# Performance work log

Measured on AMD Instinct MI355X. Metric: run time of the kernel, lower is better.

The kernel has to match this reference:

```python
import jax, jax.numpy as jnp
import numpy as np
from jax import lax
from jax.scipy.special import logsumexp

B, T, C = 512, 512, 64


def setup_inputs() -> dict:
    key = jax.random.key(0)
    k1, k2, k3, k4, k5 = jax.random.split(key, 5)
    emissions = jax.random.normal(k1, (B, T, C), dtype=jnp.float32)
    tags = jax.random.randint(k2, (B, T), 0, C, dtype=jnp.int32)
    mask = jnp.ones((B, T), dtype=jnp.int32)
    transitions = jax.random.normal(k3, (C, C), dtype=jnp.float32)
    start_transitions = jax.random.normal(k4, (C,), dtype=jnp.float32)
    end_transitions = jax.random.normal(k5, (C,), dtype=jnp.float32)
    return {"emissions": emissions, "tags": tags, "mask": mask,
            "transitions": transitions, "start_transitions": start_transitions,
            "end_transitions": end_transitions}


def _log_partition(emissions, maskb, transitions, start_transitions, end_transitions):
    # forward algorithm: lp [B,C] carried over T-1 steps
    lp0 = start_transitions[None, :] + emissions[:, 0]  # [B,C]

    def step(lp, xs):
        emit_t, mask_t = xs  # [B,C], [B]
        # score[b,i,j] = lp[b,i] + trans[i,j] + emit[b,j]
        score = lp[:, :, None] + transitions[None, :, :] + emit_t[:, None, :]
        lp_next = logsumexp(score, axis=1)  # [B,C]
        lp = jnp.where(mask_t[:, None], lp_next, lp)
        return lp, None

    xs = (jnp.swapaxes(emissions[:, 1:], 0, 1), jnp.swapaxes(maskb[:, 1:], 0, 1))
    lp, _ = lax.scan(step, lp0, xs)
    return logsumexp(lp + end_transitions[None, :], axis=1)  # [B]


def _joint_score(emissions, tags, mask, maskb, transitions, start_transitions, end_transitions):
    b_idx = jnp.arange(emissions.shape[0])
    score0 = start_transitions[tags[:, 0]] + emissions[b_idx, 0, tags[:, 0]]  # [B]
    trans = transitions[tags[:, :-1], tags[:, 1:]]  # [B,T-1]
    emit = jnp.take_along_axis(emissions, tags[:, :, None], axis=2)[:, :, 0]  # [B,T]
    step_scores = jnp.where(maskb[:, 1:], trans + emit[:, 1:], 0.0)
    last_idx = jnp.sum(mask, axis=1).astype(jnp.int32) - 1
    last_tags = tags[b_idx, last_idx]
    return score0 + jnp.sum(step_scores, axis=1) + end_transitions[last_tags]


def reference(emissions, tags, mask, transitions, start_transitions, end_transitions):
    maskb = mask.astype(bool)
    log_denominator = _log_partition(emissions, maskb, transitions, start_transitions, end_transitions)
    log_numerator = _joint_score(emissions, tags, mask, maskb, transitions, start_transitions, end_transitions)
    return jnp.mean(log_denominator - log_numerator)
```

## Files before the change

kernel.cpp:

```cpp
#include <hip/hip_runtime.h>

#define Bn 512
#define Tn 512
#define Cn 64


template <int CTRL>
__device__ __forceinline__ float fmax_dpp(const float v) {
    const int o = __builtin_amdgcn_update_dpp(__float_as_int(v), __float_as_int(v),
                                              CTRL, 0xF, 0xF, false);
    return fmaxf(v, __int_as_float(o));
}

__device__ __forceinline__ float wave_max64(float v) {
    v = fmax_dpp<0x0B1>(v);
    v = fmax_dpp<0x04E>(v);
    v = fmax_dpp<0x141>(v);
    v = fmax_dpp<0x140>(v);
    v = fmax_dpp<0x142>(v);
    v = fmax_dpp<0x143>(v);
    return __int_as_float(__builtin_amdgcn_readlane(__float_as_int(v), 63));
}

__global__ __launch_bounds__(64) void crf_half_kernel(
    const float* __restrict__ emissions,
    const int*   __restrict__ tags,
    const int*   __restrict__ mask,
    const float* __restrict__ transitions,
    const float* __restrict__ start_t,
    const float* __restrict__ end_t,
    float*       __restrict__ ws_alpha,
    float*       __restrict__ ws_beta,
    float*       __restrict__ ws_lsF,
    float*       __restrict__ ws_lsB,
    float*       __restrict__ ws_num)
{
    const int  blk = blockIdx.x;
    const bool fwd = blk < Bn;
    const int  bt  = blk & (Bn - 1);
    const int  j   = threadIdx.x;

    const float* em  = emissions + (size_t)bt * Tn * Cn + j;
    const float* em0 = emissions + (size_t)bt * Tn * Cn;
    const int*   mk  = mask + bt * Tn;
    const int*   tg  = tags + bt * Tn;

    if (fwd) {
        float nsum = 0.f;
        int   mcnt = 0;
        for (int t = j; t < Tn; t += 64) {
            const int tag_t = tg[t];
            const int m_t   = mk[t];
            mcnt += m_t;
            if (t >= 1 && m_t) {
                const int tag_p = tg[t - 1];
                nsum += transitions[tag_p * Cn + tag_t] + em0[t * Cn + tag_t];
            }
        }
#pragma unroll
        for (int off = 32; off > 0; off >>= 1) {
            nsum += __shfl_xor(nsum, off, 64);
            mcnt += __shfl_xor(mcnt, off, 64);
        }

        float w[Cn];
#pragma unroll
        for (int i = 0; i < Cn; ++i) w[i] = __expf(transitions[i * Cn + j]);

        float lp0 = start_t[j] + em[0];
        const float m0 = wave_max64(lp0);
        float log_scale = m0;
        float a_self = __expf(lp0 - m0);

        float cur_e[4];
        int   cur_m[4];
#pragma unroll
        for (int k = 0; k < 4; ++k) {
            cur_e[k] = em[(size_t)(1 + k) * Cn];
            cur_m[k] = mk[1 + k];
        }

        for (int g = 0; g < 64; ++g) {
            float nxt_e[4];
            int   nxt_m[4];
#pragma unroll
            for (int k = 0; k < 4; ++k) {
                const int t = 4 * g + 5 + k;
                nxt_e[k] = em[(size_t)t * Cn];
                nxt_m[k] = mk[t];
            }
            float ex[4];
#pragma unroll
            for (int k = 0; k < 4; ++k) ex[k] = __expf(cur_e[k]);

#pragma unroll
            for (int k = 0; k < 4; ++k) {
                float au[Cn];
#pragma unroll
                for (int i = 0; i < Cn; ++i)
                    au[i] = __int_as_float(
                        __builtin_amdgcn_readlane(__float_as_int(a_self), i));

                float acc0 = 0.f, acc1 = 0.f, acc2 = 0.f, acc3 = 0.f;
#pragma unroll
                for (int i = 0; i < Cn; i += 4) {
                    acc0 = fmaf(au[i + 0], w[i + 0], acc0);
                    acc1 = fmaf(au[i + 1], w[i + 1], acc1);
                    acc2 = fmaf(au[i + 2], w[i + 2], acc2);
                    acc3 = fmaf(au[i + 3], w[i + 3], acc3);
                }
                float s = ((acc0 + acc1) + (acc2 + acc3)) * ex[k];
                if (!cur_m[k]) s = a_self;
                if (k == 3) {
                    const float mx = wave_max64(s);
                    s *= __builtin_amdgcn_rcpf(mx);
                    log_scale += __logf(mx);
                }
                a_self = s;
            }
#pragma unroll
            for (int k = 0; k < 4; ++k) {
                cur_e[k] = nxt_e[k];
                cur_m[k] = nxt_m[k];
            }
        }

        ws_alpha[bt * Cn + j] = a_self;
        if (j == 0) {
            ws_lsF[bt] = log_scale;
            const int t0 = tg[0];
            const int tl = tg[mcnt - 1];
            ws_num[bt] = start_t[t0] + em0[t0] + nsum + end_t[tl];
        }
    } else {
        float w[Cn];
#pragma unroll
        for (int i = 0; i < Cn; ++i) w[i] = __expf(transitions[j * Cn + i]);

        float lp0 = end_t[j];
        const float m0 = wave_max64(lp0);
        float log_scale = m0;
        float b_self = __expf(lp0 - m0);

        float cur_e[4];
        int   cur_m[4];
#pragma unroll
        for (int k = 0; k < 4; ++k) {
            const int u = Tn - 1 - k;
            cur_e[k] = em[(size_t)u * Cn];
            cur_m[k] = mk[u];
        }

        for (int g = 0; g < 64; ++g) {
            float nxt_e[4];
            int   nxt_m[4];
#pragma unroll
            for (int k = 0; k < 4; ++k) {
                const int u = Tn - 5 - 4 * g - k;
                nxt_e[k] = em[(size_t)u * Cn];
                nxt_m[k] = mk[u];
            }
            float ex[4];
#pragma unroll
            for (int k = 0; k < 4; ++k) ex[k] = __expf(cur_e[k]);

#pragma unroll
            for (int k = 0; k < 4; ++k) {
                const int s_idx = 4 * g + k;
                if (s_idx < Tn / 2 - 1) {
                    const float wv = b_self * ex[k];
                    float au[Cn];
#pragma unroll
                    for (int i = 0; i < Cn; ++i)
                        au[i] = __int_as_float(
                            __builtin_amdgcn_readlane(__float_as_int(wv), i));

                    float acc0 = 0.f, acc1 = 0.f, acc2 = 0.f, acc3 = 0.f;
#pragma unroll
                    for (int i = 0; i < Cn; i += 4) {
                        acc0 = fmaf(au[i + 0], w[i + 0], acc0);
                        acc1 = fmaf(au[i + 1], w[i + 1], acc1);
                        acc2 = fmaf(au[i + 2], w[i + 2], acc2);
                        acc3 = fmaf(au[i + 3], w[i + 3], acc3);
                    }
                    float s = ((acc0 + acc1) + (acc2 + acc3));
                    if (!cur_m[k]) s = b_self;
                    if (k == 3) {
                        const float mx = wave_max64(s);
                        s *= __builtin_amdgcn_rcpf(mx);
                        log_scale += __logf(mx);
                    }
                    b_self = s;
                }
            }
#pragma unroll
            for (int k = 0; k < 4; ++k) {
                cur_e[k] = nxt_e[k];
                cur_m[k] = nxt_m[k];
            }
        }

        ws_beta[bt * Cn + j] = b_self;
        if (j == 0) ws_lsB[bt] = log_scale;
    }
}

__global__ __launch_bounds__(64) void crf_combine_kernel(
    const float* __restrict__ ws_alpha,
    const float* __restrict__ ws_beta,
    const float* __restrict__ ws_lsF,
    const float* __restrict__ ws_lsB,
    const float* __restrict__ ws_num,
    float*       __restrict__ out)
{
    const int bt = blockIdx.x;
    const int j  = threadIdx.x;
    float v = ws_alpha[bt * Cn + j] * ws_beta[bt * Cn + j];
#pragma unroll
    for (int off = 32; off > 0; off >>= 1) v += __shfl_xor(v, off, 64);
    if (j == 0) {
        const float denom = ws_lsF[bt] + ws_lsB[bt] + __logf(v);
        atomicAdd(out, (denom - ws_num[bt]) * (1.0f / Bn));
    }
}

__global__ void crf_zero_kernel(float* out) { out[0] = 0.f; }

extern "C" void kernel_launch(void* const* d_in, const int* in_sizes, int n_in,
                              void* d_out, int out_size, void* d_ws, size_t ws_size,
                              hipStream_t stream)
{
    const float* emissions   = (const float*)d_in[0];
    const int*   tags        = (const int*)d_in[1];
    const int*   mask        = (const int*)d_in[2];
    const float* transitions = (const float*)d_in[3];
    const float* start_t     = (const float*)d_in[4];
    const float* end_t       = (const float*)d_in[5];

    float* ws       = (float*)d_ws;
    float* ws_alpha = ws;
    float* ws_beta  = ws_alpha + Bn * Cn;
    float* ws_lsF   = ws_beta + Bn * Cn;
    float* ws_lsB   = ws_lsF + Bn;
    float* ws_num   = ws_lsB + Bn;

    crf_zero_kernel<<<1, 1, 0, stream>>>((float*)d_out);
    crf_half_kernel<<<2 * Bn, Cn, 0, stream>>>(emissions, tags, mask, transitions,
                                               start_t, end_t,
                                               ws_alpha, ws_beta, ws_lsF, ws_lsB, ws_num);
    crf_combine_kernel<<<Bn, Cn, 0, stream>>>(ws_alpha, ws_beta, ws_lsF, ws_lsB,
                                              ws_num, (float*)d_out);
}
```

Baseline: 173.0 us.

## Broadcast state via LDS vector loads and packed FMA instead of readlane

Replaces the 64 per-step readlanes, which broadcast the scaled alpha/beta vector across the wave, with a write to a double-buffered LDS array followed by 16-byte broadcast reads. The dot product now uses packed two-wide FMAs on float2 vectors, and the renormalisation multiply is deferred into the next step's k==0 multiply. This aims to cut scalar readlane serialization and halve FMA issue count. The cost is LDS round-trip latency on the serial recurrence, plus reliance on wave_barrier alone for intra-wave ordering.

```diff
diff --git a/kernel.cpp b/kernel.cpp
--- a/kernel.cpp
+++ b/kernel.cpp
@@ -4,6 +4,9 @@
 #define Tn 512
 #define Cn 64
 
+
+typedef float f2 __attribute__((ext_vector_type(2)));
+typedef float f4 __attribute__((ext_vector_type(4)));
 
 template <int CTRL>
 __device__ __forceinline__ float fmax_dpp(const float v) {
@@ -40,6 +43,8 @@
     const int  bt  = blk & (Bn - 1);
     const int  j   = threadIdx.x;
 
+    __shared__ __align__(16) float abuf[2][Cn];
+
     const float* em  = emissions + (size_t)bt * Tn * Cn + j;
     const float* em0 = emissions + (size_t)bt * Tn * Cn;
     const int*   mk  = mask + bt * Tn;
@@ -63,14 +68,18 @@
             mcnt += __shfl_xor(mcnt, off, 64);
         }
 
-        float w[Cn];
-#pragma unroll
-        for (int i = 0; i < Cn; ++i) w[i] = __expf(transitions[i * Cn + j]);
+        f2 wv[32];
+#pragma unroll
+        for (int p = 0; p < 32; ++p) {
+            wv[p][0] = __expf(transitions[(2 * p)     * Cn + j]);
+            wv[p][1] = __expf(transitions[(2 * p + 1) * Cn + j]);
+        }
 
         float lp0 = start_t[j] + em[0];
         const float m0 = wave_max64(lp0);
         float log_scale = m0;
         float a_self = __expf(lp0 - m0);
+        float c_pend = 1.0f;
 
         float cur_e[4];
         int   cur_m[4];
@@ -95,25 +104,35 @@
 
 #pragma unroll
             for (int k = 0; k < 4; ++k) {
-                float au[Cn];
-#pragma unroll
-                for (int i = 0; i < Cn; ++i)
-                    au[i] = __int_as_float(
-                        __builtin_amdgcn_readlane(__float_as_int(a_self), i));
-
-                float acc0 = 0.f, acc1 = 0.f, acc2 = 0.f, acc3 = 0.f;
-#pragma unroll
-                for (int i = 0; i < Cn; i += 4) {
-                    acc0 = fmaf(au[i + 0], w[i + 0], acc0);
-                    acc1 = fmaf(au[i + 1], w[i + 1], acc1);
-                    acc2 = fmaf(au[i + 2], w[i + 2], acc2);
-                    acc3 = fmaf(au[i + 3], w[i + 3], acc3);
-                }
-                float s = ((acc0 + acc1) + (acc2 + acc3)) * ex[k];
+                abuf[k & 1][j] = a_self;
+                __builtin_amdgcn_wave_barrier();
+
+                const f4* ap = (const f4*)abuf[k & 1];
+                f2 facc0 = {0.f, 0.f}, facc1 = {0.f, 0.f};
+                f2 facc2 = {0.f, 0.f}, facc3 = {0.f, 0.f};
+#pragma unroll
+                for (int p = 0; p < 16; ++p) {
+                    const f4 q = ap[p];
+                    const f2 lo = {q.x, q.y};
+                    const f2 hi = {q.z, q.w};
+                    if ((p & 1) == 0) {
+                        facc0 = __builtin_elementwise_fma(lo, wv[2 * p],     facc0);
+                        facc1 = __builtin_elementwise_fma(hi, wv[2 * p + 1], facc1);
+                    } else {
+                        facc2 = __builtin_elementwise_fma(lo, wv[2 * p],     facc2);
+                        facc3 = __builtin_elementwise_fma(hi, wv[2 * p + 1], facc3);
+                    }
+                }
+                const f2 rr = (facc0 + facc2) + (facc1 + facc3);
+                float s = (rr.x + rr.y) * ex[k];
                 if (!cur_m[k]) s = a_self;
+                if (k == 0) {
+                    s *= c_pend;
+                    c_pend = 1.0f;
+                }
                 if (k == 3) {
                     const float mx = wave_max64(s);
-                    s *= __builtin_amdgcn_rcpf(mx);
+                    c_pend = __builtin_amdgcn_rcpf(mx);
                     log_scale += __logf(mx);
                 }
                 a_self = s;
@@ -125,6 +144,7 @@
             }
         }
 
+        a_self *= c_pend;
         ws_alpha[bt * Cn + j] = a_self;
         if (j == 0) {
             ws_lsF[bt] = log_scale;
@@ -133,14 +153,18 @@
             ws_num[bt] = start_t[t0] + em0[t0] + nsum + end_t[tl];
         }
     } else {
-        float w[Cn];
-#pragma unroll
-        for (int i = 0; i < Cn; ++i) w[i] = __expf(transitions[j * Cn + i]);
+        f2 wv[32];
+#pragma unroll
+        for (int p = 0; p < 32; ++p) {
+            wv[p][0] = __expf(transitions[j * Cn + 2 * p]);
+            wv[p][1] = __expf(transitions[j * Cn + 2 * p + 1]);
+        }
 
         float lp0 = end_t[j];
         const float m0 = wave_max64(lp0);
         float log_scale = m0;
         float b_self = __expf(lp0 - m0);
+        float c_pend = 1.0f;
 
         float cur_e[4];
         int   cur_m[4];
@@ -168,26 +192,36 @@
             for (int k = 0; k < 4; ++k) {
                 const int s_idx = 4 * g + k;
                 if (s_idx < Tn / 2 - 1) {
-                    const float wv = b_self * ex[k];
-                    float au[Cn];
-#pragma unroll
-                    for (int i = 0; i < Cn; ++i)
-                        au[i] = __int_as_float(
-                            __builtin_amdgcn_readlane(__float_as_int(wv), i));
-
-                    float acc0 = 0.f, acc1 = 0.f, acc2 = 0.f, acc3 = 0.f;
-#pragma unroll
-                    for (int i = 0; i < Cn; i += 4) {
-                        acc0 = fmaf(au[i + 0], w[i + 0], acc0);
-                        acc1 = fmaf(au[i + 1], w[i + 1], acc1);
-                        acc2 = fmaf(au[i + 2], w[i + 2], acc2);
-                        acc3 = fmaf(au[i + 3], w[i + 3], acc3);
-                    }
-                    float s = ((acc0 + acc1) + (acc2 + acc3));
+                    const float wval = b_self * ex[k];
+                    abuf[k & 1][j] = wval;
+                    __builtin_amdgcn_wave_barrier();
+
+                    const f4* ap = (const f4*)abuf[k & 1];
+                    f2 facc0 = {0.f, 0.f}, facc1 = {0.f, 0.f};
+                    f2 facc2 = {0.f, 0.f}, facc3 = {0.f, 0.f};
+#pragma unroll
+                    for (int p = 0; p < 16; ++p) {
+                        const f4 q = ap[p];
+                        const f2 lo = {q.x, q.y};
+                        const f2 hi = {q.z, q.w};
+                        if ((p & 1) == 0) {
+                            facc0 = __builtin_elementwise_fma(lo, wv[2 * p],     facc0);
+                            facc1 = __builtin_elementwise_fma(hi, wv[2 * p + 1], facc1);
+                        } else {
+                            facc2 = __builtin_elementwise_fma(lo, wv[2 * p],     facc2);
+                            facc3 = __builtin_elementwise_fma(hi, wv[2 * p + 1], facc3);
+                        }
+                    }
+                    const f2 rr = (facc0 + facc2) + (facc1 + facc3);
+                    float s = rr.x + rr.y;
                     if (!cur_m[k]) s = b_self;
+                    if (k == 0) {
+                        s *= c_pend;
+                        c_pend = 1.0f;
+                    }
                     if (k == 3) {
                         const float mx = wave_max64(s);
-                        s *= __builtin_amdgcn_rcpf(mx);
+                        c_pend = __builtin_amdgcn_rcpf(mx);
                         log_scale += __logf(mx);
                     }
                     b_self = s;
@@ -200,6 +234,7 @@
             }
         }
 
+        b_self *= c_pend;
         ws_beta[bt * Cn + j] = b_self;
         if (j == 0) ws_lsB[bt] = log_scale;
     }
```

New measurement: 225.7 us. 1.3x slower.

## Batch 16 sequences per wave and run CRF forward/backward recursion on bf16 MFMA

Applied to the files above, without the earlier changes.

Replaces the per-sequence readlane/FMA matrix-vector recursion with a batched 16x64 by 64x64 product using bf16 MFMA instructions. The exponentiated transition matrix is split into hi and lo bf16 parts to recover precision, with alpha staged through LDS between steps. The numerator computation moves into the combine kernel, and the output zeroing is folded into the main kernel, removing one launch. This cuts the 64-readlane-per-step serial cost and launches far fewer waves, at the price of bf16 rounding of alpha, LDS round trips every step, and lower occupancy (64 waves).

```diff
diff --git a/kernel.cpp b/kernel.cpp
--- a/kernel.cpp
+++ b/kernel.cpp
@@ -3,228 +3,455 @@
 #define Bn 512
 #define Tn 512
 #define Cn 64
-
+#define NCH 16
+#define NGRP (Bn / NCH)
+#define LDP 20
+
+
+typedef float f4    __attribute__((ext_vector_type(4)));
+typedef short bfrag __attribute__((ext_vector_type(8)));
+typedef unsigned int u32x4 __attribute__((ext_vector_type(4)));
+
+static __device__ __forceinline__ unsigned int pkbf16(float a, float b) {
+    unsigned int r;
+    asm("v_cvt_pk_bf16_f32 %0, %1, %2" : "=v"(r) : "v"(a), "v"(b));
+    return r;
+}
 
 template <int CTRL>
-__device__ __forceinline__ float fmax_dpp(const float v) {
+static __device__ __forceinline__ float fmax_dpp(const float v) {
     const int o = __builtin_amdgcn_update_dpp(__float_as_int(v), __float_as_int(v),
                                               CTRL, 0xF, 0xF, false);
     return fmaxf(v, __int_as_float(o));
 }
-
-__device__ __forceinline__ float wave_max64(float v) {
+static __device__ __forceinline__ float rowmax16(float v) {
     v = fmax_dpp<0x0B1>(v);
     v = fmax_dpp<0x04E>(v);
     v = fmax_dpp<0x141>(v);
     v = fmax_dpp<0x140>(v);
-    v = fmax_dpp<0x142>(v);
-    v = fmax_dpp<0x143>(v);
-    return __int_as_float(__builtin_amdgcn_readlane(__float_as_int(v), 63));
-}
-
-__global__ __launch_bounds__(64) void crf_half_kernel(
+    return v;
+}
+static __device__ __forceinline__ f4 mfma16(bfrag a, bfrag b, f4 c) {
+    return __builtin_amdgcn_mfma_f32_16x16x32_bf16(a, b, c, 0, 0, 0);
+}
+
+__global__ __launch_bounds__(64)
+__attribute__((amdgpu_waves_per_eu(1, 1)))
+void crf_mfma_kernel(const float* __restrict__ emissions,
+                     const int*   __restrict__ mask,
+                     const float* __restrict__ transitions,
+                     const float* __restrict__ start_t,
+                     const float* __restrict__ end_t,
+                     float*       __restrict__ ws_alpha,
+                     float*       __restrict__ ws_beta,
+                     float*       __restrict__ ws_lsF,
+                     float*       __restrict__ ws_lsB,
+                     float*       __restrict__ out)
+{
+    const int  blk = blockIdx.x;
+    const bool fwd = blk < NGRP;
+    const int  b0  = (fwd ? blk : blk - NGRP) * NCH;
+    const int  l   = threadIdx.x;
+    const int  lg  = l >> 4;
+    const int  lo4 = l & 15;
+
+    if (blk == 0 && l == 0) out[0] = 0.f;
+
+    __shared__ __align__(16) float lT[Cn * Cn];
+    __shared__ __align__(16) float lA[2][Cn * LDP];
+    __shared__ float sc[NCH];
+
+    {
+        const f4* T4  = (const f4*)transitions;
+        f4*       lT4 = (f4*)lT;
+#pragma unroll
+        for (int q = 0; q < 16; ++q) lT4[q * 64 + l] = T4[q * 64 + l];
+    }
+    __builtin_amdgcn_wave_barrier();
+
+    bfrag whi[4][2], wlo[4][2];
+#pragma unroll
+    for (int n0 = 0; n0 < 4; ++n0)
+#pragma unroll
+        for (int kh = 0; kh < 2; ++kh) {
+            float wv[8];
+#pragma unroll
+            for (int ii = 0; ii < 8; ++ii) {
+                const int kk = kh * 32 + lg * 8 + ii;
+                const int jj = n0 * 16 + lo4;
+                wv[ii] = __expf(fwd ? lT[kk * Cn + jj] : lT[jj * Cn + kk]);
+            }
+            u32x4 H, L;
+#pragma unroll
+            for (int p = 0; p < 4; ++p) {
+                const unsigned int h = pkbf16(wv[2*p], wv[2*p+1]);
+                const float h0 = __uint_as_float((h & 0xffffu) << 16);
+                const float h1 = __uint_as_float(h & 0xffff0000u);
+                H[p] = h;
+                L[p] = pkbf16(wv[2*p] - h0, wv[2*p+1] - h1);
+            }
+            whi[n0][kh] = __builtin_bit_cast(bfrag, H);
+            wlo[n0][kh] = __builtin_bit_cast(bfrag, L);
+        }
+
+    const f4* em4 = (const f4*)(emissions + (size_t)(b0 + lo4) * Tn * Cn + lg * 8);
+    float ls[4];
+    bfrag a0, a1;
+    const f4 zz = {0.f, 0.f, 0.f, 0.f};
+
+    if (fwd) {
+        {
+            float v[16];
+#pragma unroll
+            for (int z = 0; z < 4; ++z) {
+                const f4 e = em4[(z >> 1) * 8 + (z & 1)];
+#pragma unroll
+                for (int q = 0; q < 4; ++q)
+                    v[z*4+q] = start_t[(z>>1)*32 + lg*8 + (z&1)*4 + q] + e[q];
+            }
+            float mx = v[0];
+#pragma unroll
+            for (int i2 = 1; i2 < 16; ++i2) mx = fmaxf(mx, v[i2]);
+            mx = fmaxf(mx, __int_as_float(__builtin_amdgcn_ds_swizzle(__float_as_int(mx), 0x401F)));
+            mx = fmaxf(mx, __shfl_xor(mx, 32, 64));
+            u32x4 A0, A1;
+#pragma unroll
+            for (int p = 0; p < 4; ++p) {
+                A0[p] = pkbf16(__expf(v[2*p]   - mx), __expf(v[2*p+1]   - mx));
+                A1[p] = pkbf16(__expf(v[8+2*p] - mx), __expf(v[8+2*p+1] - mx));
+            }
+            a0 = __builtin_bit_cast(bfrag, A0);
+            a1 = __builtin_bit_cast(bfrag, A1);
+            if (l < NCH) sc[l] = mx;
+        }
+        __builtin_amdgcn_wave_barrier();
+#pragma unroll
+        for (int r = 0; r < 4; ++r) ls[r] = sc[4*lg + r];
+
+        f4  eq0[4], eq1[4];
+        int mv0, mv1;
+#pragma unroll
+        for (int z = 0; z < 4; ++z) {
+            eq1[z] = em4[1*16 + (z>>1)*8 + (z&1)];
+            eq0[z] = em4[2*16 + (z>>1)*8 + (z&1)];
+        }
+        mv1 = 1; if (l < NCH) mv1 = mask[(b0 + l) * Tn + 1];
+        mv0 = 1; if (l < NCH) mv0 = mask[(b0 + l) * Tn + 2];
+
+        unsigned long long mwlast = ~0ull;
+
+#pragma unroll 1
+        for (int t = 1; t <= 256; ++t) {
+            const int par = t & 1;
+            const f4 pfa = em4[(t+2)*16 + 0];
+            const f4 pfb = em4[(t+2)*16 + 1];
+            const f4 pfc = em4[(t+2)*16 + 8];
+            const f4 pfd = em4[(t+2)*16 + 9];
+            int pfm = 1; if (l < NCH) pfm = mask[(b0 + l) * Tn + (t + 2)];
+
+            f4 acc0 = mfma16(a0, whi[0][0], zz);
+            f4 acc1 = mfma16(a0, whi[1][0], zz);
+            f4 acc2 = mfma16(a0, whi[2][0], zz);
+            f4 acc3 = mfma16(a0, whi[3][0], zz);
+            acc0 = mfma16(a1, whi[0][1], acc0);
+            acc1 = mfma16(a1, whi[1][1], acc1);
+            acc2 = mfma16(a1, whi[2][1], acc2);
+            acc3 = mfma16(a1, whi[3][1], acc3);
+            acc0 = mfma16(a0, wlo[0][0], acc0);
+            acc1 = mfma16(a0, wlo[1][0], acc1);
+            acc2 = mfma16(a0, wlo[2][0], acc2);
+            acc3 = mfma16(a0, wlo[3][0], acc3);
+            acc0 = mfma16(a1, wlo[0][1], acc0);
+            acc1 = mfma16(a1, wlo[1][1], acc1);
+            acc2 = mfma16(a1, wlo[2][1], acc2);
+            acc3 = mfma16(a1, wlo[3][1], acc3);
+
+            const unsigned long long mw = __ballot((par ? mv1 : mv0) != 0);
+            const bool all1 = (mw == ~0ull);
+            mwlast = mw;
+
+            if ((t & 3) == 0) {
+#pragma unroll
+                for (int r = 0; r < 4; ++r) {
+                    float mr = fmaxf(fmaxf(acc0[r], acc1[r]), fmaxf(acc2[r], acc3[r]));
+                    mr = rowmax16(mr);
+                    float scl = __builtin_amdgcn_rcpf(mr);
+                    float lga = __logf(mr);
+                    if (!all1) {
+                        const bool fz = !((mw >> (4*lg + r)) & 1);
+                        scl = fz ? 1.0f : scl;
+                        lga = fz ? 0.0f : lga;
+                    }
+                    ls[r] += lga;
+                    acc0[r] *= scl; acc1[r] *= scl; acc2[r] *= scl; acc3[r] *= scl;
+                }
+            }
+
+            *(f4*)&lA[par][(     lo4) * LDP + 4*lg] = acc0;
+            *(f4*)&lA[par][(16 + lo4) * LDP + 4*lg] = acc1;
+            *(f4*)&lA[par][(32 + lo4) * LDP + 4*lg] = acc2;
+            *(f4*)&lA[par][(48 + lo4) * LDP + 4*lg] = acc3;
+            __builtin_amdgcn_wave_barrier();
+
+            if (t != 256) {
+                float ex[16];
+#pragma unroll
+                for (int z = 0; z < 4; ++z) {
+                    const f4 e = par ? eq1[z] : eq0[z];
+#pragma unroll
+                    for (int q = 0; q < 4; ++q) ex[z*4+q] = __expf(e[q]);
+                }
+                u32x4 NA0, NA1;
+#pragma unroll
+                for (int p = 0; p < 4; ++p) {
+                    const float f0 = lA[par][(     lg*8 + 2*p    ) * LDP + lo4] * ex[2*p];
+                    const float f1 = lA[par][(     lg*8 + 2*p + 1) * LDP + lo4] * ex[2*p+1];
+                    const float f2 = lA[par][(32 + lg*8 + 2*p    ) * LDP + lo4] * ex[8+2*p];
+                    const float f3 = lA[par][(32 + lg*8 + 2*p + 1) * LDP + lo4] * ex[8+2*p+1];
+                    NA0[p] = pkbf16(f0, f1);
+                    NA1[p] = pkbf16(f2, f3);
+                }
+                if (!all1) {
+                    const bool fz = !((mw >> lo4) & 1);
+                    const u32x4 O0 = __builtin_bit_cast(u32x4, a0);
+                    const u32x4 O1 = __builtin_bit_cast(u32x4, a1);
+#pragma unroll
+                    for (int p = 0; p < 4; ++p) {
+                        NA0[p] = fz ? O0[p] : NA0[p];
+                        NA1[p] = fz ? O1[p] : NA1[p];
+                    }
+                }
+                a0 = __builtin_bit_cast(bfrag, NA0);
+                a1 = __builtin_bit_cast(bfrag, NA1);
+                if (par) { eq1[0]=pfa; eq1[1]=pfb; eq1[2]=pfc; eq1[3]=pfd; mv1 = pfm; }
+                else     { eq0[0]=pfa; eq0[1]=pfb; eq0[2]=pfc; eq0[3]=pfd; mv0 = pfm; }
+            }
+        }
+
+        __builtin_amdgcn_wave_barrier();
+#pragma unroll
+        for (int s = 0; s < 16; ++s) {
+            const int i2 = (s >> 3) * 32 + lg * 8 + (s & 7);
+            ws_alpha[(size_t)(b0 + lo4) * Cn + i2] = lA[0][i2 * LDP + lo4];
+        }
+        if (mwlast != ~0ull) {
+            asm volatile("s_waitcnt vmcnt(0)" ::: "memory");
+            const bool fz = !((mwlast >> lo4) & 1);
+            if (fz) {
+                const u32x4 U0 = __builtin_bit_cast(u32x4, a0);
+                const u32x4 U1 = __builtin_bit_cast(u32x4, a1);
+#pragma unroll
+                for (int s = 0; s < 16; ++s) {
+                    const int kh = s >> 3, ii = s & 7;
+                    const unsigned int w = (kh == 0) ? U0[ii >> 1] : U1[ii >> 1];
+                    const float av = __uint_as_float(((w >> (16 * (ii & 1))) & 0xffffu) << 16);
+                    const f4 e = (s < 8) ? ((ii < 4) ? eq0[0] : eq0[1])
+                                         : ((ii < 4) ? eq0[2] : eq0[3]);
+                    const float ev = e[ii & 3];
+                    const int i2 = kh * 32 + lg * 8 + ii;
+                    ws_alpha[(size_t)(b0 + lo4) * Cn + i2] = av * __expf(0.f - ev);
+                }
+            }
+        }
+        if (lo4 == 0) {
+#pragma unroll
+            for (int r = 0; r < 4; ++r) ws_lsF[b0 + 4*lg + r] = ls[r];
+        }
+    } else {
+        {
+            float v[16], bv[16];
+#pragma unroll
+            for (int z = 0; z < 4; ++z) {
+                const f4 e = em4[511*16 + (z>>1)*8 + (z&1)];
+#pragma unroll
+                for (int q = 0; q < 4; ++q) {
+                    const int i2 = (z>>1)*32 + lg*8 + (z&1)*4 + q;
+                    bv[z*4+q] = end_t[i2];
+                    v[z*4+q]  = bv[z*4+q] + e[q];
+                }
+            }
+            float mx = v[0];
+#pragma unroll
+            for (int i2 = 1; i2 < 16; ++i2) mx = fmaxf(mx, v[i2]);
+            mx = fmaxf(mx, __int_as_float(__builtin_amdgcn_ds_swizzle(__float_as_int(mx), 0x401F)));
+            mx = fmaxf(mx, __shfl_xor(mx, 32, 64));
+            u32x4 A0, A1;
+#pragma unroll
+            for (int p = 0; p < 4; ++p) {
+                A0[p] = pkbf16(__expf(v[2*p]   - mx), __expf(v[2*p+1]   - mx));
+                A1[p] = pkbf16(__expf(v[8+2*p] - mx), __expf(v[8+2*p+1] - mx));
+            }
+            a0 = __builtin_bit_cast(bfrag, A0);
+            a1 = __builtin_bit_cast(bfrag, A1);
+            if (l < NCH) sc[l] = mx;
+#pragma unroll
+            for (int s = 0; s < 16; ++s) {
+                const int i2 = (s >> 3) * 32 + lg * 8 + (s & 7);
+                lA[1][i2 * LDP + lo4] = __expf(bv[s] - mx);
+            }
+        }
+        __builtin_amdgcn_wave_barrier();
+#pragma unroll
+        for (int r = 0; r < 4; ++r) ls[r] = sc[4*lg + r];
+
+        f4  eq0[4], eq1[4];
+        int mv0, mv1;
+#pragma unroll
+        for (int z = 0; z < 4; ++z) {
+            eq0[z] = em4[510*16 + (z>>1)*8 + (z&1)];
+            eq1[z] = em4[509*16 + (z>>1)*8 + (z&1)];
+        }
+        mv0 = 1; if (l < NCH) mv0 = mask[(b0 + l) * Tn + 511];
+        mv1 = 1; if (l < NCH) mv1 = mask[(b0 + l) * Tn + 510];
+
+#pragma unroll 1
+        for (int s = 0; s < 255; ++s) {
+            const int par = s & 1;
+            const f4 pfa = em4[(508 - s)*16 + 0];
+            const f4 pfb = em4[(508 - s)*16 + 1];
+            const f4 pfc = em4[(508 - s)*16 + 8];
+            const f4 pfd = em4[(508 - s)*16 + 9];
+            int pfm = 1; if (l < NCH) pfm = mask[(b0 + l) * Tn + (509 - s)];
+
+            f4 acc0 = mfma16(a0, whi[0][0], zz);
+            f4 acc1 = mfma16(a0, whi[1][0], zz);
+            f4 acc2 = mfma16(a0, whi[2][0], zz);
+            f4 acc3 = mfma16(a0, whi[3][0], zz);
+            acc0 = mfma16(a1, whi[0][1], acc0);
+            acc1 = mfma16(a1, whi[1][1], acc1);
+            acc2 = mfma16(a1, whi[2][1], acc2);
+            acc3 = mfma16(a1, whi[3][1], acc3);
+            acc0 = mfma16(a0, wlo[0][0], acc0);
+            acc1 = mfma16(a0, wlo[1][0], acc1);
+            acc2 = mfma16(a0, wlo[2][0], acc2);
+            acc3 = mfma16(a0, wlo[3][0], acc3);
+            acc0 = mfma16(a1, wlo[0][1], acc0);
+            acc1 = mfma16(a1, wlo[1][1], acc1);
+            acc2 = mfma16(a1, wlo[2][1], acc2);
+            acc3 = mfma16(a1, wlo[3][1], acc3);
+
+            const unsigned long long mw = __ballot((par ? mv1 : mv0) != 0);
+            const bool all1 = (mw == ~0ull);
+
+            if ((s & 3) == 3) {
+#pragma unroll
+                for (int r = 0; r < 4; ++r) {
+                    float mr = fmaxf(fmaxf(acc0[r], acc1[r]), fmaxf(acc2[r], acc3[r]));
+                    mr = rowmax16(mr);
+                    float scl = __builtin_amdgcn_rcpf(mr);
+                    float lga = __logf(mr);
+                    if (!all1) {
+                        const bool fz = !((mw >> (4*lg + r)) & 1);
+                        scl = fz ? 1.0f : scl;
+                        lga = fz ? 0.0f : lga;
+                    }
+                    ls[r] += lga;
+                    acc0[r] *= scl; acc1[r] *= scl; acc2[r] *= scl; acc3[r] *= scl;
+                }
+            }
+
+            if (!all1) {
+                const f4 pv0 = *(const f4*)&lA[par ^ 1][(     lo4) * LDP + 4*lg];
+                const f4 pv1 = *(const f4*)&lA[par ^ 1][(16 + lo4) * LDP + 4*lg];
+                const f4 pv2 = *(const f4*)&lA[par ^ 1][(32 + lo4) * LDP + 4*lg];
+                const f4 pv3 = *(const f4*)&lA[par ^ 1][(48 + lo4) * LDP + 4*lg];
+#pragma unroll
+                for (int r = 0; r < 4; ++r) {
+                    const bool fz = !((mw >> (4*lg + r)) & 1);
+                    acc0[r] = fz ? pv0[r] : acc0[r];
+                    acc1[r] = fz ? pv1[r] : acc1[r];
+                    acc2[r] = fz ? pv2[r] : acc2[r];
+                    acc3[r] = fz ? pv3[r] : acc3[r];
+                }
+            }
+            *(f4*)&lA[par][(     lo4) * LDP + 4*lg] = acc0;
+            *(f4*)&lA[par][(16 + lo4) * LDP + 4*lg] = acc1;
+            *(f4*)&lA[par][(32 + lo4) * LDP + 4*lg] = acc2;
+            *(f4*)&lA[par][(48 + lo4) * LDP + 4*lg] = acc3;
+            __builtin_amdgcn_wave_barrier();
+
+            if (s != 254) {
+                float ex[16];
+#pragma unroll
+                for (int z = 0; z < 4; ++z) {
+                    const f4 e = par ? eq1[z] : eq0[z];
+#pragma unroll
+                    for (int q = 0; q < 4; ++q) ex[z*4+q] = __expf(e[q]);
+                }
+                u32x4 NA0, NA1;
+#pragma unroll
+                for (int p = 0; p < 4; ++p) {
+                    const float f0 = lA[par][(     lg*8 + 2*p    ) * LDP + lo4] * ex[2*p];
+                    const float f1 = lA[par][(     lg*8 + 2*p + 1) * LDP + lo4] * ex[2*p+1];
+                    const float f2 = lA[par][(32 + lg*8 + 2*p    ) * LDP + lo4] * ex[8+2*p];
+                    const float f3 = lA[par][(32 + lg*8 + 2*p + 1) * LDP + lo4] * ex[8+2*p+1];
+                    NA0[p] = pkbf16(f0, f1);
+                    NA1[p] = pkbf16(f2, f3);
+                }
+                a0 = __builtin_bit_cast(bfrag, NA0);
+                a1 = __builtin_bit_cast(bfrag, NA1);
+                if (par) { eq1[0]=pfa; eq1[1]=pfb; eq1[2]=pfc; eq1[3]=pfd; mv1 = pfm; }
+                else     { eq0[0]=pfa; eq0[1]=pfb; eq0[2]=pfc; eq0[3]=pfd; mv0 = pfm; }
+            }
+        }
+
+        __builtin_amdgcn_wave_barrier();
+#pragma unroll
+        for (int s = 0; s < 16; ++s) {
+            const int i2 = (s >> 3) * 32 + lg * 8 + (s & 7);
+            ws_beta[(size_t)(b0 + lo4) * Cn + i2] = lA[0][i2 * LDP + lo4];
+        }
+        if (lo4 == 0) {
+#pragma unroll
+            for (int r = 0; r < 4; ++r) ws_lsB[b0 + 4*lg + r] = ls[r];
+        }
+    }
+}
+
+__global__ __launch_bounds__(64) void crf_combine_kernel(
     const float* __restrict__ emissions,
     const int*   __restrict__ tags,
     const int*   __restrict__ mask,
     const float* __restrict__ transitions,
     const float* __restrict__ start_t,
     const float* __restrict__ end_t,
-    float*       __restrict__ ws_alpha,
-    float*       __restrict__ ws_beta,
-    float*       __restrict__ ws_lsF,
-    float*       __restrict__ ws_lsB,
-    float*       __restrict__ ws_num)
-{
-    const int  blk = blockIdx.x;
-    const bool fwd = blk < Bn;
-    const int  bt  = blk & (Bn - 1);
-    const int  j   = threadIdx.x;
-
-    const float* em  = emissions + (size_t)bt * Tn * Cn + j;
-    const float* em0 = emissions + (size_t)bt * Tn * Cn;
-    const int*   mk  = mask + bt * Tn;
-    const int*   tg  = tags + bt * Tn;
-
-    if (fwd) {
-        float nsum = 0.f;
-        int   mcnt = 0;
-        for (int t = j; t < Tn; t += 64) {
-            const int tag_t = tg[t];
-            const int m_t   = mk[t];
-            mcnt += m_t;
-            if (t >= 1 && m_t) {
-                const int tag_p = tg[t - 1];
-                nsum += transitions[tag_p * Cn + tag_t] + em0[t * Cn + tag_t];
-            }
-        }
-#pragma unroll
-        for (int off = 32; off > 0; off >>= 1) {
-            nsum += __shfl_xor(nsum, off, 64);
-            mcnt += __shfl_xor(mcnt, off, 64);
-        }
-
-        float w[Cn];
-#pragma unroll
-        for (int i = 0; i < Cn; ++i) w[i] = __expf(transitions[i * Cn + j]);
-
-        float lp0 = start_t[j] + em[0];
-        const float m0 = wave_max64(lp0);
-        float log_scale = m0;
-        float a_self = __expf(lp0 - m0);
-
-        float cur_e[4];
-        int   cur_m[4];
-#pragma unroll
-        for (int k = 0; k < 4; ++k) {
-            cur_e[k] = em[(size_t)(1 + k) * Cn];
-            cur_m[k] = mk[1 + k];
-        }
-
-        for (int g = 0; g < 64; ++g) {
-            float nxt_e[4];
-            int   nxt_m[4];
-#pragma unroll
-            for (int k = 0; k < 4; ++k) {
-                const int t = 4 * g + 5 + k;
-                nxt_e[k] = em[(size_t)t * Cn];
-                nxt_m[k] = mk[t];
-            }
-            float ex[4];
-#pragma unroll
-            for (int k = 0; k < 4; ++k) ex[k] = __expf(cur_e[k]);
-
-#pragma unroll
-            for (int k = 0; k < 4; ++k) {
-                float au[Cn];
-#pragma unroll
-                for (int i = 0; i < Cn; ++i)
-                    au[i] = __int_as_float(
-                        __builtin_amdgcn_readlane(__float_as_int(a_self), i));
-
-                float acc0 = 0.f, acc1 = 0.f, acc2 = 0.f, acc3 = 0.f;
-#pragma unroll
-                for (int i = 0; i < Cn; i += 4) {
-                    acc0 = fmaf(au[i + 0], w[i + 0], acc0);
-                    acc1 = fmaf(au[i + 1], w[i + 1], acc1);
-                    acc2 = fmaf(au[i + 2], w[i + 2], acc2);
-                    acc3 = fmaf(au[i + 3], w[i + 3], acc3);
-                }
-                float s = ((acc0 + acc1) + (acc2 + acc3)) * ex[k];
-                if (!cur_m[k]) s = a_self;
-                if (k == 3) {
-                    const float mx = wave_max64(s);
-                    s *= __builtin_amdgcn_rcpf(mx);
-                    log_scale += __logf(mx);
-                }
-                a_self = s;
-            }
-#pragma unroll
-            for (int k = 0; k < 4; ++k) {
-                cur_e[k] = nxt_e[k];
-                cur_m[k] = nxt_m[k];
-            }
-        }
-
-        ws_alpha[bt * Cn + j] = a_self;
-        if (j == 0) {
-            ws_lsF[bt] = log_scale;
-            const int t0 = tg[0];
-            const int tl = tg[mcnt - 1];
-            ws_num[bt] = start_t[t0] + em0[t0] + nsum + end_t[tl];
-        }
-    } else {
-        float w[Cn];
-#pragma unroll
-        for (int i = 0; i < Cn; ++i) w[i] = __expf(transitions[j * Cn + i]);
-
-        float lp0 = end_t[j];
-        const float m0 = wave_max64(lp0);
-        float log_scale = m0;
-        float b_self = __expf(lp0 - m0);
-
-        float cur_e[4];
-        int   cur_m[4];
-#pragma unroll
-        for (int k = 0; k < 4; ++k) {
-            const int u = Tn - 1 - k;
-            cur_e[k] = em[(size_t)u * Cn];
-            cur_m[k] = mk[u];
-        }
-
-        for (int g = 0; g < 64; ++g) {
-            float nxt_e[4];
-            int   nxt_m[4];
-#pragma unroll
-            for (int k = 0; k < 4; ++k) {
-                const int u = Tn - 5 - 4 * g - k;
-                nxt_e[k] = em[(size_t)u * Cn];
-                nxt_m[k] = mk[u];
-            }
-            float ex[4];
-#pragma unroll
-            for (int k = 0; k < 4; ++k) ex[k] = __expf(cur_e[k]);
-
-#pragma unroll
-            for (int k = 0; k < 4; ++k) {
-                const int s_idx = 4 * g + k;
-                if (s_idx < Tn / 2 - 1) {
-                    const float wv = b_self * ex[k];
-                    float au[Cn];
-#pragma unroll
-                    for (int i = 0; i < Cn; ++i)
-                        au[i] = __int_as_float(
-                            __builtin_amdgcn_readlane(__float_as_int(wv), i));
-
-                    float acc0 = 0.f, acc1 = 0.f, acc2 = 0.f, acc3 = 0.f;
-#pragma unroll
-                    for (int i = 0; i < Cn; i += 4) {
-                        acc0 = fmaf(au[i + 0], w[i + 0], acc0);
-                        acc1 = fmaf(au[i + 1], w[i + 1], acc1);
-                        acc2 = fmaf(au[i + 2], w[i + 2], acc2);
-                        acc3 = fmaf(au[i + 3], w[i + 3], acc3);
-                    }
-                    float s = ((acc0 + acc1) + (acc2 + acc3));
-                    if (!cur_m[k]) s = b_self;
-                    if (k == 3) {
-                        const float mx = wave_max64(s);
-                        s *= __builtin_amdgcn_rcpf(mx);
-                        log_scale += __logf(mx);
-                    }
-                    b_self = s;
-                }
-            }
-#pragma unroll
-            for (int k = 0; k < 4; ++k) {
-                cur_e[k] = nxt_e[k];
-                cur_m[k] = nxt_m[k];
-            }
-        }
-
-        ws_beta[bt * Cn + j] = b_self;
-        if (j == 0) ws_lsB[bt] = log_scale;
-    }
-}
-
-__global__ __launch_bounds__(64) void crf_combine_kernel(
     const float* __restrict__ ws_alpha,
     const float* __restrict__ ws_beta,
     const float* __restrict__ ws_lsF,
     const float* __restrict__ ws_lsB,
-    const float* __restrict__ ws_num,
     float*       __restrict__ out)
 {
     const int bt = blockIdx.x;
     const int j  = threadIdx.x;
-    float v = ws_alpha[bt * Cn + j] * ws_beta[bt * Cn + j];
+    const float* em0 = emissions + (size_t)bt * Tn * Cn;
+    const int*   tg  = tags + bt * Tn;
+    const int*   mk  = mask + bt * Tn;
+
+    float nsum = 0.f;
+    int   mcnt = 0;
+    for (int t = j; t < Tn; t += 64) {
+        const int tag_t = tg[t];
+        const int m_t   = mk[t];
+        mcnt += m_t;
+        if (t >= 1 && m_t)
+            nsum += transitions[tg[t-1] * Cn + tag_t] + em0[t * Cn + tag_t];
+    }
+#pragma unroll
+    for (int off = 32; off > 0; off >>= 1) {
+        nsum += __shfl_xor(nsum, off, 64);
+        mcnt += __shfl_xor(mcnt, off, 64);
+    }
+
+    float v = ws_alpha[bt * Cn + j] * __expf(em0[256 * Cn + j]) * ws_beta[bt * Cn + j];
 #pragma unroll
     for (int off = 32; off > 0; off >>= 1) v += __shfl_xor(v, off, 64);
+
     if (j == 0) {
+        const float num   = start_t[tg[0]] + em0[tg[0]] + nsum + end_t[tg[mcnt - 1]];
         const float denom = ws_lsF[bt] + ws_lsB[bt] + __logf(v);
-        atomicAdd(out, (denom - ws_num[bt]) * (1.0f / Bn));
+        atomicAdd(out, (denom - num) * (1.0f / Bn));
     }
 }
-
-__global__ void crf_zero_kernel(float* out) { out[0] = 0.f; }
 
 extern "C" void kernel_launch(void* const* d_in, const int* in_sizes, int n_in,
                               void* d_out, int out_size, void* d_ws, size_t ws_size,
@@ -242,12 +469,13 @@
     float* ws_beta  = ws_alpha + Bn * Cn;
     float* ws_lsF   = ws_beta + Bn * Cn;
     float* ws_lsB   = ws_lsF + Bn;
-    float* ws_num   = ws_lsB + Bn;
-
-    crf_zero_kernel<<<1, 1, 0, stream>>>((float*)d_out);
-    crf_half_kernel<<<2 * Bn, Cn, 0, stream>>>(emissions, tags, mask, transitions,
-                                               start_t, end_t,
-                                               ws_alpha, ws_beta, ws_lsF, ws_lsB, ws_num);
-    crf_combine_kernel<<<Bn, Cn, 0, stream>>>(ws_alpha, ws_beta, ws_lsF, ws_lsB,
-                                              ws_num, (float*)d_out);
-}
+
+    crf_mfma_kernel<<<2 * NGRP, 64, 0, stream>>>(emissions, mask, transitions,
+                                                 start_t, end_t,
+                                                 ws_alpha, ws_beta, ws_lsF, ws_lsB,
+                                                 (float*)d_out);
+    crf_combine_kernel<<<Bn, 64, 0, stream>>>(emissions, tags, mask, transitions,
+                                              start_t, end_t,
+                                              ws_alpha, ws_beta, ws_lsF, ws_lsB,
+                                              (float*)d_out);
+}
```

After: 386.8 us. +123.6%, slower.
